# Optimization experiments

Hardware: AMD Instinct MI355X
Metric: run time of the kernel (lower is better)

## Reference

```python
import jax, jax.numpy as jnp
import numpy as np

N = 100000
E = 3200000
D = 128


def setup_inputs() -> dict:
    key = jax.random.key(0)
    k1, k2, k3, k4 = jax.random.split(key, 4)
    x = jax.random.normal(k1, (N, D), dtype=jnp.float32)
    edge_index = jax.random.randint(k2, (2, E), 0, N, dtype=jnp.int64)
    W1 = jax.random.normal(k3, (D, 16), dtype=jnp.float32) * (1.0 / np.sqrt(D))
    b1 = jnp.zeros((16,), dtype=jnp.float32)
    W2 = jax.random.normal(k4, (16, 2), dtype=jnp.float32) * (1.0 / np.sqrt(16))
    b2 = jnp.zeros((2,), dtype=jnp.float32)
    return {"x": x, "edge_index": edge_index, "W1": W1, "b1": b1, "W2": W2, "b2": b2}


def _gcn_conv(h, src, dst, norm, W, b):
    # transform first (out_dim <= in_dim), then normalized scatter-add aggregation
    h = h @ W                                   # [N, out]
    msg = h[src] * norm[:, None]                # [E+N, out] gathered messages
    agg = jax.ops.segment_sum(msg, dst, num_segments=N)
    return agg + b


def reference(x, edge_index, W1, b1, W2, b2):
    loops = jnp.arange(N, dtype=edge_index.dtype)
    src = jnp.concatenate([edge_index[0], loops])   # row (message source)
    dst = jnp.concatenate([edge_index[1], loops])   # col (aggregation target)
    # symmetric GCN normalization: deg over dst, norm = d^-1/2[src] * d^-1/2[dst]
    deg = jax.ops.segment_sum(jnp.ones_like(src, dtype=x.dtype), dst, num_segments=N)
    dinv = jnp.where(deg > 0, jax.lax.rsqrt(deg), 0.0)
    norm = dinv[src] * dinv[dst]

    h = _gcn_conv(x, src, dst, norm, W1, b1)
    h = jax.nn.relu(h)
    h = _gcn_conv(h, src, dst, norm, W2, b2)
    return jax.nn.log_softmax(h, axis=1)
```

## Files before the change

### kernel.cpp

```cpp
#include <hip/hip_runtime.h>
#include <hip/hip_fp16.h>
#include <math.h>

#define N_NODES 100000
#define N_EDGES 3200000
#define D_IN    128
#define H1      16

#define BSH   8
#define NPB   256
#define NB    391
#define CAP   9216
#define PBLK  512
#define CHUNK 6250
#define MROWS 64


__global__ __launch_bounds__(512) void k_zero(int* __restrict__ cursor) {
    int t = threadIdx.x;
    if (t < NB) cursor[t] = 0;
}

__global__ __launch_bounds__(512) void k_partition(const int* __restrict__ ei,
                                                   int* __restrict__ cursor,
                                                   unsigned int* __restrict__ eop) {
    __shared__ int h[NB];
    __shared__ int resv[NB];
    __shared__ unsigned char rank8[CHUNK];
    int t = threadIdx.x;
    for (int i = t; i < NB; i += 512) h[i] = 0;
    __syncthreads();
    int c0 = blockIdx.x * CHUNK;
    const int* srcs = ei + c0;
    const int* dsts = ei + N_EDGES + c0;
    for (int i = t; i < CHUNK; i += 512)
        rank8[i] = (unsigned char)atomicAdd(&h[dsts[i] >> BSH], 1);
    __syncthreads();
    for (int b = t; b < NB; b += 512) {
        int c = h[b];
        resv[b] = c ? atomicAdd(&cursor[b], c) : 0;
    }
    __syncthreads();
    for (int i = t; i < CHUNK; i += 512) {
        int s = srcs[i];
        int d = dsts[i];
        int b = d >> BSH;
        int pos = resv[b] + (int)rank8[i];
        if (pos < CAP)
            eop[(size_t)b * CAP + pos] = ((unsigned)s << BSH) | (unsigned)(d & (NPB - 1));
    }
}

__global__ __launch_bounds__(512) void k_build(const int* __restrict__ cursor,
                                               unsigned int* __restrict__ eop,
                                               int* __restrict__ nstart,
                                               int* __restrict__ ndeg,
                                               float* __restrict__ dinv) {
    __shared__ unsigned int els[CAP];
    __shared__ int cnt[NPB];
    __shared__ int off[NPB];
    int t = threadIdx.x, b = blockIdx.x;
    if (t < NPB) cnt[t] = 0;
    __syncthreads();
    int n = cursor[b]; if (n > CAP) n = CAP;
    unsigned int* reg = eop + (size_t)b * CAP;
    for (int i = t; i < n; i += 512) {
        unsigned int v = reg[i];
        int r = atomicAdd(&cnt[v & (NPB - 1)], 1);
        els[i] = v | ((unsigned)(r & 127) << 25);
    }
    __syncthreads();
    int val = (t < NPB) ? cnt[t] : 0;
    if (t < NPB) off[t] = val;
    __syncthreads();
    for (int o = 1; o < NPB; o <<= 1) {
        int u = 0;
        if (t < NPB && t >= o) u = off[t - o];
        __syncthreads();
        if (t < NPB) off[t] += u;
        __syncthreads();
    }
    if (t < NPB) {
        int ex = off[t] - val;
        int node = (b << BSH) + t;
        if (node < N_NODES) {
            nstart[node] = b * CAP + ex;
            ndeg[node]   = val;
            dinv[node]   = rsqrtf((float)(val + 1));
        }
        off[t] = ex;
    }
    __syncthreads();
    for (int i = t; i < n; i += 512) {
        unsigned int u = els[i];
        int dloc = u & (NPB - 1);
        int r    = (u >> 25) & 127;
        reg[off[dloc] + r] = (u >> BSH) & 0x1FFFF;
    }
}

__global__ __launch_bounds__(256) void k_mm1(const float* __restrict__ x,
                                             const float* __restrict__ W1,
                                             const float* __restrict__ dinv,
                                             __half* __restrict__ h1h) {
    __shared__ float sX[MROWS][D_IN + 1];
    int t = threadIdx.x;
    int r0 = blockIdx.x * MROWS;
    for (int i = t; i < MROWS * (D_IN / 4); i += 256) {
        int row = i >> 5, c4 = i & 31;
        int grow = r0 + row;
        float4 v = (grow < N_NODES) ? ((const float4*)x)[(size_t)grow * 32 + c4]
                                    : make_float4(0.f, 0.f, 0.f, 0.f);
        sX[row][c4 * 4 + 0] = v.x; sX[row][c4 * 4 + 1] = v.y;
        sX[row][c4 * 4 + 2] = v.z; sX[row][c4 * 4 + 3] = v.w;
    }
    __syncthreads();
    int lane = t & 63;
    int c0 = __builtin_amdgcn_readfirstlane((t >> 6) * 4);
    float a0 = 0.f, a1 = 0.f, a2 = 0.f, a3 = 0.f;
#pragma unroll 4
    for (int d = 0; d < D_IN; ++d) {
        float xv = sX[lane][d];
        a0 = fmaf(xv, W1[d * 16 + c0 + 0], a0);
        a1 = fmaf(xv, W1[d * 16 + c0 + 1], a1);
        a2 = fmaf(xv, W1[d * 16 + c0 + 2], a2);
        a3 = fmaf(xv, W1[d * 16 + c0 + 3], a3);
    }
    int grow = r0 + lane;
    if (grow < N_NODES) {
        float di = dinv[grow];
        __half2* o = (__half2*)(h1h + (size_t)grow * H1 + c0);
        o[0] = __floats2half2_rn(a0 * di, a1 * di);
        o[1] = __floats2half2_rn(a2 * di, a3 * di);
    }
}

__global__ __launch_bounds__(256) void k_agg1(const unsigned int* __restrict__ eop,
                                              const int* __restrict__ nstart,
                                              const int* __restrict__ ndeg,
                                              const __half* __restrict__ h1h,
                                              const float* __restrict__ dinv,
                                              const float* __restrict__ b1,
                                              const float* __restrict__ W2,
                                              float2* __restrict__ h2f) {
    int t = threadIdx.x;
    int g = t >> 4, l = t & 15;
    int node = blockIdx.x * 16 + g;
    int e0 = nstart[node], e1 = e0 + ndeg[node];
    float acc = 0.f;
    int j = e0;
    for (; j + 4 <= e1; j += 4) {
        int s0 = eop[j], s1 = eop[j + 1], s2 = eop[j + 2], s3 = eop[j + 3];
        acc += __half2float(h1h[s0 * H1 + l]) + __half2float(h1h[s1 * H1 + l])
             + __half2float(h1h[s2 * H1 + l]) + __half2float(h1h[s3 * H1 + l]);
    }
    for (; j < e1; ++j) acc += __half2float(h1h[(int)eop[j] * H1 + l]);
    float di = dinv[node];
    float s  = acc + __half2float(h1h[node * H1 + l]);
    float h  = fmaxf(fmaf(di, s, b1[l]), 0.f);
    float p0 = h * W2[2 * l], p1 = h * W2[2 * l + 1];
#pragma unroll
    for (int off = 1; off < 16; off <<= 1) {
        p0 += __shfl_xor(p0, off);
        p1 += __shfl_xor(p1, off);
    }
    if (l == 0) h2f[node] = make_float2(p0 * di, p1 * di);
}

__global__ __launch_bounds__(256) void k_agg2(const unsigned int* __restrict__ eop,
                                              const int* __restrict__ nstart,
                                              const int* __restrict__ ndeg,
                                              const float2* __restrict__ h2f,
                                              const float* __restrict__ dinv,
                                              const float* __restrict__ b2,
                                              float* __restrict__ out) {
    int tg = blockIdx.x * 256 + threadIdx.x;
    int node = tg >> 2, l = tg & 3;
    if (node >= N_NODES) return;
    int e0 = nstart[node], e1 = e0 + ndeg[node];
    float ax = 0.f, ay = 0.f;
    for (int j = e0 + l; j < e1; j += 4) {
        float2 m = h2f[eop[j]];
        ax += m.x; ay += m.y;
    }
    ax += __shfl_xor(ax, 1); ay += __shfl_xor(ay, 1);
    ax += __shfl_xor(ax, 2); ay += __shfl_xor(ay, 2);
    if (l == 0) {
        float di = dinv[node];
        float2 self = h2f[node];
        float a0 = fmaf(di, ax + self.x, b2[0]);
        float a1 = fmaf(di, ay + self.y, b2[1]);
        float m  = fmaxf(a0, a1);
        float lg = logf(expf(a0 - m) + expf(a1 - m));
        out[2 * node]     = a0 - m - lg;
        out[2 * node + 1] = a1 - m - lg;
    }
}

extern "C" void kernel_launch(void* const* d_in, const int* in_sizes, int n_in,
                              void* d_out, int out_size, void* d_ws, size_t ws_size,
                              hipStream_t stream) {
    const float* x  = (const float*)d_in[0];
    const int*   ei = (const int*)d_in[1];
    const float* W1 = (const float*)d_in[2];
    const float* b1 = (const float*)d_in[3];
    const float* W2 = (const float*)d_in[4];
    const float* b2 = (const float*)d_in[5];
    float* out = (float*)d_out;

    int*          cursor = (int*)d_ws;
    int*          nstart = cursor + 512;
    int*          ndeg   = nstart + 100352;
    float*        dinv   = (float*)(ndeg + 100352);
    __half*       h1h    = (__half*)(dinv + 100352);
    float2*       h2f    = (float2*)(h1h + (size_t)100352 * H1);
    unsigned int* eop    = (unsigned int*)(h2f + 100352);

    k_zero     <<<1,    512, 0, stream>>>(cursor);
    k_partition<<<PBLK, 512, 0, stream>>>(ei, cursor, eop);
    k_build    <<<NB,   512, 0, stream>>>(cursor, eop, nstart, ndeg, dinv);
    k_mm1      <<<(N_NODES + MROWS - 1) / MROWS, 256, 0, stream>>>(x, W1, dinv, h1h);
    k_agg1     <<<N_NODES / 16, 256, 0, stream>>>(eop, nstart, ndeg, h1h, dinv, b1, W2, h2f);
    k_agg2     <<<(N_NODES * 4 + 255) / 256, 256, 0, stream>>>(eop, nstart, ndeg, h2f, dinv, b2, out);
}
```

Measured before the change: 231.7 us.

## Stage partitioned edges in LDS and write padded contiguous bucket runs

The partition kernel now places each chunk's edges into a shared-memory buffer grouped by bucket, with each bucket's run padded to a multiple of 16. It then copies the buffer out to global memory in contiguous runs instead of scattering single edges, which is meant to replace many uncoalesced global writes. The padding slots hold a sentinel value that the build kernel skips. The build kernel now assigns slots with a second round of shared atomics rather than packed ranks, so edge order within a node can vary. In exchange, CAP grows and both kernels use more shared memory, which may lower occupancy.

Result: faster. 222.6 us (-3.9%).

```diff
diff --git a/kernel.cpp b/kernel.cpp
--- a/kernel.cpp
+++ b/kernel.cpp
@@ -7,13 +7,15 @@
 #define D_IN    128
 #define H1      16
 
-#define BSH   8
-#define NPB   256
-#define NB    391
-#define CAP   9216
-#define PBLK  512
-#define CHUNK 6250
-#define MROWS 64
+#define BSH     8
+#define NPB     256
+#define NB      391
+#define CAP     13056
+#define PBLK    512
+#define CHUNK   6250
+#define ELS_CAP 12128
+#define NLINES  (ELS_CAP / 16)
+#define MROWS   64
 
 
 __global__ __launch_bounds__(512) void k_zero(int* __restrict__ cursor) {
@@ -24,11 +26,14 @@
 __global__ __launch_bounds__(512) void k_partition(const int* __restrict__ ei,
                                                    int* __restrict__ cursor,
                                                    unsigned int* __restrict__ eop) {
-    __shared__ int h[NB];
+    __shared__ int h[512];
+    __shared__ int loff[512];
     __shared__ int resv[NB];
+    __shared__ unsigned short owner[NLINES];
     __shared__ unsigned char rank8[CHUNK];
-    int t = threadIdx.x;
-    for (int i = t; i < NB; i += 512) h[i] = 0;
+    __shared__ unsigned int els[ELS_CAP];
+    int t = threadIdx.x;
+    h[t] = 0;
     __syncthreads();
     int c0 = blockIdx.x * CHUNK;
     const int* srcs = ei + c0;
@@ -36,18 +41,39 @@
     for (int i = t; i < CHUNK; i += 512)
         rank8[i] = (unsigned char)atomicAdd(&h[dsts[i] >> BSH], 1);
     __syncthreads();
-    for (int b = t; b < NB; b += 512) {
-        int c = h[b];
-        resv[b] = c ? atomicAdd(&cursor[b], c) : 0;
-    }
+    int cp = (h[t] + 15) & ~15;
+    loff[t] = cp;
+    __syncthreads();
+    for (int o = 1; o < 512; o <<= 1) {
+        int u = (t >= o) ? loff[t - o] : 0;
+        __syncthreads();
+        loff[t] += u;
+        __syncthreads();
+    }
+    int inc = loff[t];
+    int totalpad = loff[511];
+    int ex = inc - cp;
+    __syncthreads();
+    loff[t] = ex;
+    if (t < NB && cp) {
+        resv[t] = atomicAdd(&cursor[t], cp);
+        int l0 = ex >> 4;
+        for (int k = 0; k < (cp >> 4); ++k) owner[l0 + k] = (unsigned short)t;
+    }
+    for (int i = t; i < totalpad; i += 512) els[i] = 0xFFFFFFFFu;
     __syncthreads();
     for (int i = t; i < CHUNK; i += 512) {
         int s = srcs[i];
         int d = dsts[i];
         int b = d >> BSH;
-        int pos = resv[b] + (int)rank8[i];
+        els[loff[b] + (int)rank8[i]] = ((unsigned)s << BSH) | (unsigned)(d & (NPB - 1));
+    }
+    __syncthreads();
+    for (int i = t; i < totalpad; i += 512) {
+        int b   = owner[i >> 4];
+        int pos = resv[b] + (i - loff[b]);
         if (pos < CAP)
-            eop[(size_t)b * CAP + pos] = ((unsigned)s << BSH) | (unsigned)(d & (NPB - 1));
+            eop[(size_t)b * CAP + pos] = els[i];
     }
 }
 
@@ -59,6 +85,7 @@
     __shared__ unsigned int els[CAP];
     __shared__ int cnt[NPB];
     __shared__ int off[NPB];
+    __shared__ int cur[NPB];
     int t = threadIdx.x, b = blockIdx.x;
     if (t < NPB) cnt[t] = 0;
     __syncthreads();
@@ -66,8 +93,8 @@
     unsigned int* reg = eop + (size_t)b * CAP;
     for (int i = t; i < n; i += 512) {
         unsigned int v = reg[i];
-        int r = atomicAdd(&cnt[v & (NPB - 1)], 1);
-        els[i] = v | ((unsigned)(r & 127) << 25);
+        els[i] = v;
+        if ((int)v >= 0) atomicAdd(&cnt[v & (NPB - 1)], 1);
     }
     __syncthreads();
     int val = (t < NPB) ? cnt[t] : 0;
@@ -88,14 +115,15 @@
             ndeg[node]   = val;
             dinv[node]   = rsqrtf((float)(val + 1));
         }
-        off[t] = ex;
+        cur[t] = ex;
     }
     __syncthreads();
     for (int i = t; i < n; i += 512) {
-        unsigned int u = els[i];
-        int dloc = u & (NPB - 1);
-        int r    = (u >> 25) & 127;
-        reg[off[dloc] + r] = (u >> BSH) & 0x1FFFF;
+        unsigned int v = els[i];
+        if ((int)v >= 0) {
+            int r = atomicAdd(&cur[v & (NPB - 1)], 1);
+            reg[r] = v >> BSH;
+        }
     }
 }
 
```
